# Optimization experiments

Hardware: AMD Instinct MI355X
Metric: run time of the kernel (lower is better)

The kernel has to match this reference:

```python
import jax, jax.numpy as jnp
import numpy as np

N, E, O, C, D_IN, OUT, L, B = 10000, 80000, 10, 64, 16, 16, 2, 16
DEG, WIDEN, BD = 3, 4, 64
EPS = 1e-6


def fibonacci_sphere(n):
    # deterministic near-uniform grid of n unit vectors on S^2 (stands in for GridGenerator's repulsion grid)
    i = jnp.arange(n, dtype=jnp.float32) + 0.5
    phi = jnp.arccos(1.0 - 2.0 * i / n)
    theta = jnp.pi * (1.0 + 5.0 ** 0.5) * i
    return jnp.stack([jnp.cos(theta) * jnp.sin(phi), jnp.sin(theta) * jnp.sin(phi), jnp.cos(phi)], axis=-1)


def poly_features(x, degree):
    # PolynomialFeatures: concat x, x(x)x, x(x)x(x)x, ... flattened outer products
    feats = [x]
    cur = x
    for _ in range(degree):
        cur = (cur[..., :, None] * x[..., None, :]).reshape(x.shape[:-1] + (-1,))
        feats.append(cur)
    return jnp.concatenate(feats, axis=-1)


def layer_norm(x, scale, bias):
    mu = jnp.mean(x, axis=-1, keepdims=True)
    var = jnp.mean((x - mu) ** 2, axis=-1, keepdims=True)
    return (x - mu) * jax.lax.rsqrt(var + EPS) * scale + bias


def setup_inputs():
    key = jax.random.key(0)
    ks = jax.random.split(key, 16)
    def w(k, shape):
        return jax.random.normal(k, shape, dtype=jnp.float32) / np.sqrt(shape[-2])
    P_SP = 2 + 4 + 8 + 16  # poly features of 2-dim spatial invariants, degree 3
    P_OR = 4               # poly features of 1-dim orientation invariant, degree 3
    return {
        "x": jax.random.normal(ks[0], (N, D_IN), jnp.float32),
        "pos": jax.random.normal(ks[1], (N, 3), jnp.float32),
        "basis_w1": w(ks[2], (P_SP, C)), "basis_b1": jnp.zeros((C,), jnp.float32),
        "basis_w2": w(ks[3], (C, BD)), "basis_b2": jnp.zeros((BD,), jnp.float32),
        "fbasis_w1": w(ks[4], (P_OR, C)), "fbasis_b1": jnp.zeros((C,), jnp.float32),
        "fbasis_w2": w(ks[5], (C, BD)), "fbasis_b2": jnp.zeros((BD,), jnp.float32),
        "embed_w": w(ks[6], (D_IN, C)),
        "conv_kw": w(ks[7], (L, BD, C)),
        "conv_fw": w(ks[8], (L, BD, C)),
        "conv_b": jnp.zeros((L, C), jnp.float32),
        "norm_s": jnp.ones((L, C), jnp.float32),
        "norm_b": jnp.zeros((L, C), jnp.float32),
        "lin1_w": w(ks[9], (L, C, WIDEN * C)), "lin1_b": jnp.zeros((L, WIDEN * C), jnp.float32),
        "lin2_w": w(ks[10], (L, WIDEN * C, C)), "lin2_b": jnp.zeros((L, C), jnp.float32),
        "ro_w": w(ks[11], (L, C, OUT)), "ro_b": jnp.zeros((L, OUT), jnp.float32),
        "edge_index": jax.random.randint(ks[12], (2, E), 0, N, jnp.int32),
        "batch": jnp.sort(jax.random.randint(ks[13], (N,), 0, B, jnp.int32)),
    }


def reference(x, pos, basis_w1, basis_b1, basis_w2, basis_b2, fbasis_w1, fbasis_b1, fbasis_w2, fbasis_b2, embed_w, conv_kw, conv_fw, conv_b, norm_s, norm_b, lin1_w, lin1_b, lin2_w, lin2_b, ro_w, ro_b, edge_index, batch):
    ori = fibonacci_sphere(O)                                             # [O,3]
    send, recv = edge_index[0], edge_index[1]
    rel = (pos[send] - pos[recv])[:, None, :]                              # [E,1,3]
    inv1 = jnp.sum(rel * ori[None], axis=-1, keepdims=True)                # [E,O,1]
    inv2 = jnp.linalg.norm(rel - inv1 * ori[None], axis=-1, keepdims=True) # [E,O,1]
    inv3 = jnp.sum(ori[None, :, :] * ori[:, None, :], axis=-1, keepdims=True)  # [O,O,1]
    sp = jnp.concatenate([inv1, inv2], axis=-1)                            # [E,O,2]
    kb = jax.nn.gelu(poly_features(sp, DEG) @ basis_w1 + basis_b1)
    kb = jax.nn.gelu(kb @ basis_w2 + basis_b2)                             # [E,O,BD]
    fkb = jax.nn.gelu(poly_features(inv3, DEG) @ fbasis_w1 + fbasis_b1)
    fkb = jax.nn.gelu(fkb @ fbasis_w2 + fbasis_b2)                         # [O,O,BD]
    h = jnp.broadcast_to((x @ embed_w)[:, None, :], (N, O, C))             # [N,O,C]
    readout = jnp.zeros((N, O, OUT), h.dtype)
    for l in range(L):
        # depthwise spatial conv: gather-send, modulate by kernel, scatter-add to receivers
        msg = h[send] * (kb @ conv_kw[l])                                  # [E,O,C]
        h1 = jax.ops.segment_sum(msg, recv, num_segments=N)                # [N,O,C]
        # depthwise fiber (orientation) conv
        fk = fkb @ conv_fw[l]                                              # [O,O,C]
        h2 = jnp.einsum('noc,poc->npc', h1, fk) / O + conv_b[l]
        # ConvNeXt MLP + residual
        y = layer_norm(h2, norm_s[l], norm_b[l])
        y = jax.nn.gelu(y @ lin1_w[l] + lin1_b[l]) @ lin2_w[l] + lin2_b[l]
        h = h + y
        readout = readout + (h @ ro_w[l] + ro_b[l])
    readout = readout / L
    out_scalar = jnp.mean(readout, axis=-2)                                # [N,OUT]
    pooled = jnp.zeros((B, OUT), out_scalar.dtype).at[batch].add(out_scalar)
    return pooled
```

## Files before the change

### kernel.cpp

```cpp
#include <hip/hip_runtime.h>
#include <math.h>

#define N_   10000
#define E_   80000
#define O_   10
#define B_   16
#define OUT_ 16
#define NROW_ (N_*O_)
#define NITEM_ (E_*O_)

typedef __attribute__((ext_vector_type(8))) short bf16x8;
typedef __attribute__((ext_vector_type(4))) short bf16x4;
typedef __attribute__((ext_vector_type(4))) float f32x4;

#define MFMA16(a,b,c) __builtin_amdgcn_mfma_f32_16x16x32_bf16(a,b,c,0,0,0)

__device__ __forceinline__ float gelu_f(float x) {
    float u = fmaf(0.044715f, x * x, 1.0f);
    float e = __builtin_amdgcn_exp2f(2.3022083f * x * u);
    float r = __builtin_amdgcn_rcpf(e + 1.0f);
    return fmaf(-x, r, x);
}

__device__ __forceinline__ unsigned short f2bf(float f) {
    union { float f; unsigned int u; } v; v.f = f;
    unsigned int r = v.u + 0x7FFFu + ((v.u >> 16) & 1u);
    return (unsigned short)(r >> 16);
}
__device__ __forceinline__ float bf2f(unsigned short u) {
    union { unsigned int u; float f; } v; v.u = ((unsigned int)u) << 16;
    return v.f;
}
__device__ __forceinline__ unsigned int cvtpk(float lo, float hi) {
    unsigned int r;
    asm("v_cvt_pk_bf16_f32 %0, %1, %2" : "=v"(r) : "v"(lo), "v"(hi));
    return r;
}
__device__ __forceinline__ bf16x4 pack4(float a, float b, float c, float d) {
    union { unsigned int u[2]; bf16x4 v; } z;
    z.u[0] = cvtpk(a, b);
    z.u[1] = cvtpk(c, d);
    return z.v;
}

__device__ __forceinline__ void fib_vec(int idx, float& vx, float& vy, float& vz) {
    float i = (float)idx + 0.5f;
    float phi = acosf(1.0f - 2.0f * i / (float)O_);
    float theta = 3.14159265358979323846f * (1.0f + 2.2360679774997896964f) * i;
    float sp = sinf(phi);
    vx = cosf(theta) * sp; vy = sinf(theta) * sp; vz = cosf(phi);
}

__global__ __launch_bounds__(256) void k_pack(
    const float* __restrict__ bw1, const float* __restrict__ bw2,
    const float* __restrict__ ckw, const float* __restrict__ l1w,
    const float* __restrict__ l2w, const float* __restrict__ row_w,
    float* __restrict__ orig,
    unsigned short* __restrict__ wW1P, unsigned short* __restrict__ wW2P,
    unsigned short* __restrict__ wCKP, unsigned short* __restrict__ wL1P,
    unsigned short* __restrict__ wL2P, unsigned short* __restrict__ wROP)
{
    const int g = blockIdx.x * 256 + threadIdx.x;
    if (g < 2048) {
        int idx = g;
        int t = idx >> 9, rem = idx & 511;
        int ln = rem >> 3, j = rem & 7;
        int row = t*16 + (ln & 15);
        int k = (ln >> 4)*8 + j;
        float s = 0.0f;
        if (k < 14) {
            const int moff[14] = {0,1,2,3,5,6,7,10,13,14,15,19,25,29};
            const int mcnt[14] = {1,1,1,2,1,1,3,3,1,1,4,6,4,1};
            const int mlist[30] = {0,1,2,3,4,5,6,7,8,10,9,11,12,13,14,
                                   15,16,18,22,17,19,20,23,24,26,21,25,27,28,29};
            for (int q = 0; q < mcnt[k]; ++q) s += bw1[mlist[moff[k]+q]*64 + row];
        }
        wW1P[idx] = f2bf(s);
    } else if (g < 6144) {
        int idx = g - 2048;
        int t = idx >> 9, rem = idx & 511;
        int mt = t >> 1, ks = t & 1;
        int ln = rem >> 3, j = rem & 7;
        int row = mt*16 + (ln & 15);
        int k = ks*32 + (ln >> 4)*8 + j;
        wW2P[idx] = f2bf(bw2[k*64 + row]);
    } else if (g < 14336) {
        int idx = g - 6144;
        int l = idx >> 12, r2 = idx & 4095;
        int t = r2 >> 9, rem = r2 & 511;
        int mt = t >> 1, ks = t & 1;
        int ln = rem >> 3, j = rem & 7;
        int row = mt*16 + (ln & 15);
        int k = ks*32 + (ln >> 4)*8 + j;
        wCKP[idx] = f2bf(ckw[l*4096 + k*64 + row]);
    } else if (g < 47104) {
        int idx = g - 14336;
        int l = idx >> 14, r2 = idx & 16383;
        int t = r2 >> 9, rem = r2 & 511;
        int mt = t >> 1, ks = t & 1;
        int ln = rem >> 3, j = rem & 7;
        int row = mt*16 + (ln & 15);
        int k = ks*32 + (ln >> 4)*8 + j;
        wL1P[idx] = f2bf(l1w[l*16384 + k*256 + row]);
    } else if (g < 79872) {
        int idx = g - 47104;
        int l = idx >> 14, r2 = idx & 16383;
        int t = r2 >> 9, rem = r2 & 511;
        int mt2 = t >> 3, ksg = t & 7;
        int ln = rem >> 3, j = rem & 7;
        int row = mt2*16 + (ln & 15);
        int k = ksg*32 + (ln >> 4)*8 + j;
        wL2P[idx] = f2bf(l2w[l*16384 + k*64 + row]);
    } else if (g < 81920) {
        int idx = g - 79872;
        int l = idx >> 10, r2 = idx & 1023;
        int ks = r2 >> 9, rem = r2 & 511;
        int ln = rem >> 3, j = rem & 7;
        int row = ln & 15;
        int k = ks*32 + (ln >> 4)*8 + j;
        wROP[idx] = f2bf(row_w[l*1024 + k*16 + row]);
    } else if (g < 81920 + O_) {
        int o = g - 81920;
        float vx, vy, vz;
        fib_vec(o, vx, vy, vz);
        orig[o*3+0] = vx; orig[o*3+1] = vy; orig[o*3+2] = vz;
    }
}

__global__ __launch_bounds__(256) void k_fibpre(
    const float* __restrict__ fw1, const float* __restrict__ fb1,
    const float* __restrict__ fw2, const float* __restrict__ fb2,
    const float* __restrict__ cfw, float* __restrict__ fkg)
{
    __shared__ float sRow[4][64];
    const int wv = threadIdx.x >> 6, lane = threadIdx.x & 63;
    const int pr = blockIdx.x * 4 + wv;
    if (pr >= 100) return;
    const int i = pr / O_, j = pr % O_;
    float ix, iy, iz, jx, jy, jz;
    fib_vec(i, ix, iy, iz);
    fib_vec(j, jx, jy, jz);
    float a = ix*jx + iy*jy + iz*jz;
    float a2 = a*a, a3 = a2*a, a4 = a3*a;
    float v = fb1[lane];
    v = fmaf(a,  fw1[0*64+lane], v);
    v = fmaf(a2, fw1[1*64+lane], v);
    v = fmaf(a3, fw1[2*64+lane], v);
    v = fmaf(a4, fw1[3*64+lane], v);
    sRow[wv][lane] = gelu_f(v);
    float acc = fb2[lane];
    for (int b = 0; b < 64; ++b) acc = fmaf(sRow[wv][b], fw2[b*64+lane], acc);
    sRow[wv][lane] = gelu_f(acc);
    for (int l = 0; l < 2; ++l) {
        float s = 0.0f;
        for (int b = 0; b < 64; ++b) s = fmaf(sRow[wv][b], cfw[l*4096 + b*64 + lane], s);
        fkg[l*6400 + pr*64 + lane] = s;
    }
}

__global__ __launch_bounds__(256) void k_embed(
    const float* __restrict__ x, const float* __restrict__ ew,
    float* __restrict__ hg, unsigned short* __restrict__ hbf0)
{
    int t = blockIdx.x * 256 + threadIdx.x;
    if (t >= N_ * 64) return;
    int n = t >> 6, c = t & 63;
    float v = 0.0f;
#pragma unroll
    for (int k = 0; k < 16; ++k) v = fmaf(x[n*16+k], ew[k*64+c], v);
    int base = n * 640 + c;
#pragma unroll
    for (int o = 0; o < O_; ++o) hg[base + o*64] = v;
    hbf0[t] = f2bf(v);
}

__global__ __launch_bounds__(256) void k_hist(const int* __restrict__ ei, int* __restrict__ counts)
{
    int e = blockIdx.x * 256 + threadIdx.x;
    if (e < E_) atomicAdd(&counts[ei[E_ + e]], 1);
}

__global__ __launch_bounds__(1024) void k_scan(
    const int* __restrict__ counts, int* __restrict__ offs, int* __restrict__ cursor)
{
    __shared__ int part[1024];
    int t = threadIdx.x;
    const int CH = 10;
    int base_i = t * CH;
    int s = 0;
#pragma unroll
    for (int i = 0; i < CH; ++i) { int idx = base_i + i; if (idx < N_) s += counts[idx]; }
    part[t] = s;
    __syncthreads();
    for (int off = 1; off < 1024; off <<= 1) {
        int v = (t >= off) ? part[t - off] : 0;
        __syncthreads();
        part[t] += v;
        __syncthreads();
    }
    int run = (t > 0) ? part[t - 1] : 0;
#pragma unroll
    for (int i = 0; i < CH; ++i) {
        int idx = base_i + i;
        if (idx < N_) { offs[idx] = run; cursor[idx] = run; run += counts[idx]; }
    }
    if (t == 1023) offs[N_] = run;
}

__global__ __launch_bounds__(256) void k_scatter(
    const int* __restrict__ ei, const float* __restrict__ pos,
    int* __restrict__ cursor, int* __restrict__ csend, int* __restrict__ crecv,
    float* __restrict__ crel)
{
    int e = blockIdx.x * 256 + threadIdx.x;
    if (e >= E_) return;
    int s = ei[e], r = ei[E_ + e];
    int slot = atomicAdd(&cursor[r], 1);
    csend[slot] = s;
    crecv[slot] = r;
    crel[slot*3+0] = pos[s*3+0] - pos[r*3+0];
    crel[slot*3+1] = pos[s*3+1] - pos[r*3+1];
    crel[slot*3+2] = pos[s*3+2] - pos[r*3+2];
}

template<int KS>
__device__ __forceinline__ void loadB(
    const unsigned short* sData, int lane, bf16x8 Bf[4][KS])
{
    const int lm = lane & 15, lk = lane >> 4;
#pragma unroll
    for (int nt = 0; nt < 4; ++nt)
#pragma unroll
        for (int ks = 0; ks < KS; ++ks) {
            int r = nt*16 + lm;
            int kb = ks*64 + lk*16;
            Bf[nt][ks] = *(const bf16x8*)((const char*)sData + r*128 + (kb ^ ((r&7)<<4)));
        }
}

template<int KS, bool BIAS, bool GELU>
__device__ __forceinline__ void stageC(
    unsigned short* sData, const bf16x8 Bf[4][KS],
    const unsigned short* __restrict__ Wp, const float* __restrict__ bias, int lane)
{
    const int lm = lane & 15, lk = lane >> 4;
#pragma unroll
    for (int mt = 0; mt < 4; ++mt) {
        bf16x8 Af[KS];
#pragma unroll
        for (int ks = 0; ks < KS; ++ks)
            Af[ks] = *(const bf16x8*)(Wp + ((mt*KS + ks)*64 + lane)*8);
        f32x4 b4 = {0,0,0,0};
        if (BIAS) b4 = *(const f32x4*)(bias + mt*16 + (lk<<2));
#pragma unroll
        for (int nt = 0; nt < 4; ++nt) {
            f32x4 acc = b4;
#pragma unroll
            for (int ks = 0; ks < KS; ++ks) acc = MFMA16(Af[ks], Bf[nt][ks], acc);
            float v0 = acc[0], v1 = acc[1], v2 = acc[2], v3 = acc[3];
            if (GELU) { v0 = gelu_f(v0); v1 = gelu_f(v1); v2 = gelu_f(v2); v3 = gelu_f(v3); }
            bf16x4 pk = pack4(v0, v1, v2, v3);
            int rr = nt*16 + lm;
            int cb = mt*32 + (lk<<3);
            *(bf16x4*)((char*)sData + rr*128 + (cb ^ ((rr&7)<<4))) = pk;
        }
    }
}

__device__ __forceinline__ void phase0(
    unsigned short* sData, int slot, int oo, const float* __restrict__ crel,
    const float* __restrict__ ori, int tid)
{
    float r0 = crel[slot*3+0], r1 = crel[slot*3+1], r2 = crel[slot*3+2];
    float o0 = ori[oo*3+0], o1 = ori[oo*3+1], o2 = ori[oo*3+2];
    float a = r0*o0 + r1*o1 + r2*o2;
    float p0 = fmaf(-a, o0, r0), p1 = fmaf(-a, o1, r1), p2 = fmaf(-a, o2, r2);
    float b = sqrtf(p0*p0 + p1*p1 + p2*p2);
    float a2 = a*a, b2 = b*b, ab = a*b;
    float m[14];
    m[0]=a; m[1]=b; m[2]=a2; m[3]=ab; m[4]=b2;
    m[5]=a2*a; m[6]=a2*b; m[7]=a*b2; m[8]=b2*b;
    m[9]=a2*a2; m[10]=a2*ab; m[11]=a2*b2; m[12]=ab*b2; m[13]=b2*b2;
    unsigned int pk[16];
#pragma unroll
    for (int j = 0; j < 7; ++j) pk[j] = cvtpk(m[2*j], m[2*j+1]);
#pragma unroll
    for (int j = 7; j < 16; ++j) pk[j] = 0;
#pragma unroll
    for (int q = 0; q < 4; ++q) {
        int cb = q*16;
        *(f32x4*)((char*)sData + tid*128 + (cb ^ ((tid&7)<<4))) = ((const f32x4*)pk)[q];
    }
}

#define SCATTER_BODY(KC_EXPR)                                                        \
    int prevr = __shfl_up(rcv, 1);                                                   \
    unsigned long long bmask = __ballot(lane > 0 && rcv != prevr);                   \
    float a0=0,a1c=0,a2c=0,a3c=0,a4c=0,a5c=0,a6c=0,a7c=0,a8c=0,a9c=0;                \
    int cur = __builtin_amdgcn_readfirstlane(rcv);                                   \
    int soi = item0 % 10;                                                            \
    _Pragma("unroll")                                                                \
    for (int ch = 0; ch < 4; ++ch) {                                                 \
        unsigned short hvu[16]; float kcv[16];                                       \
        _Pragma("unroll")                                                            \
        for (int j = 0; j < 16; ++j) {                                               \
            const int i = ch*16 + j;                                                 \
            hvu[j] = hb[__builtin_amdgcn_readlane(myaddr, i)];                       \
            kcv[j] = (KC_EXPR);                                                      \
        }                                                                            \
        _Pragma("unroll")                                                            \
        for (int j = 0; j < 16; ++j) {                                               \
            const int i = ch*16 + j;                                                 \
            if (bmask & (1ull << i)) { FLUSH_RUN(cur); cur = __builtin_amdgcn_readlane(rcv, i); } \
            float mv = kcv[j] * bf2f(hvu[j]);                                        \
            if      (soi == 0) a0  += mv;                                            \
            else if (soi == 1) a1c += mv;                                            \
            else if (soi == 2) a2c += mv;                                            \
            else if (soi == 3) a3c += mv;                                            \
            else if (soi == 4) a4c += mv;                                            \
            else if (soi == 5) a5c += mv;                                            \
            else if (soi == 6) a6c += mv;                                            \
            else if (soi == 7) a7c += mv;                                            \
            else if (soi == 8) a8c += mv;                                            \
            else               a9c += mv;                                            \
            soi = (soi == 9) ? 0 : soi + 1;                                          \
        }                                                                            \
    }                                                                                \
    FLUSH_RUN(cur);

#define FLUSH_RUN(R) { float* bp = h1g + (R)*640 + lane; \
    atomicAdd(bp+0,a0); atomicAdd(bp+64,a1c); atomicAdd(bp+128,a2c); atomicAdd(bp+192,a3c); \
    atomicAdd(bp+256,a4c); atomicAdd(bp+320,a5c); atomicAdd(bp+384,a6c); atomicAdd(bp+448,a7c); \
    atomicAdd(bp+512,a8c); atomicAdd(bp+576,a9c); \
    a0=a1c=a2c=a3c=a4c=a5c=a6c=a7c=a8c=a9c=0.0f; }

template<bool L0>
__global__ __launch_bounds__(64) void k_msg(
    const unsigned short* __restrict__ hbf, float* __restrict__ h1g,
    const int* __restrict__ csend, const int* __restrict__ crecv,
    const float* __restrict__ crel, const float* __restrict__ ori,
    const unsigned short* __restrict__ wW1P, const unsigned short* __restrict__ wW2P,
    const unsigned short* __restrict__ wCKP_l,
    const float* __restrict__ bb1, const float* __restrict__ bb2)
{
    __shared__ unsigned short sData[64*64];
    const int lane = threadIdx.x;
    const int item0 = blockIdx.x * 64;
    const int item = item0 + lane;
    const int slot = item / 10;
    const int oo = item - slot * 10;
    const int snd = csend[slot];
    const int rcv = crecv[slot];
    phase0(sData, slot, oo, crel, ori, lane);
    {
        bf16x8 Bf1[4][1]; loadB<1>(sData, lane, Bf1);
        stageC<1, true, true>(sData, Bf1, wW1P, bb1, lane);
    }
    {
        bf16x8 Bf2[4][2]; loadB<2>(sData, lane, Bf2);
        stageC<2, true, true>(sData, Bf2, wW2P, bb2, lane);
    }
    {
        bf16x8 Bf3[4][2]; loadB<2>(sData, lane, Bf3);
        stageC<2, false, false>(sData, Bf3, wCKP_l, (const float*)0, lane);
    }
    const int myaddr = L0 ? (snd * 64) : ((snd * 10 + oo) * 64);
    const unsigned short* hb = hbf + lane;
    SCATTER_BODY(bf2f(*(const unsigned short*)((const char*)sData + i*128 + ((lane*2) ^ ((i&7)<<4)))))
}

__global__ __launch_bounds__(64) void k_msg0dual(
    const unsigned short* __restrict__ hbf, float* __restrict__ h1g,
    unsigned short* __restrict__ kc1g,
    const int* __restrict__ csend, const int* __restrict__ crecv,
    const float* __restrict__ crel, const float* __restrict__ ori,
    const unsigned short* __restrict__ wW1P, const unsigned short* __restrict__ wW2P,
    const unsigned short* __restrict__ wCK0, const unsigned short* __restrict__ wCK1,
    const float* __restrict__ bb1, const float* __restrict__ bb2)
{
    __shared__ unsigned short sData[64*64];
    const int lane = threadIdx.x;
    const int item0 = blockIdx.x * 64;
    const int item = item0 + lane;
    const int slot = item / 10;
    const int oo = item - slot * 10;
    const int snd = csend[slot];
    const int rcv = crecv[slot];
    phase0(sData, slot, oo, crel, ori, lane);
    {
        bf16x8 Bf1[4][1]; loadB<1>(sData, lane, Bf1);
        stageC<1, true, true>(sData, Bf1, wW1P, bb1, lane);
    }
    {
        bf16x8 Bf2[4][2]; loadB<2>(sData, lane, Bf2);
        stageC<2, true, true>(sData, Bf2, wW2P, bb2, lane);
    }
    bf16x8 Bf3[4][2]; loadB<2>(sData, lane, Bf3);
    stageC<2, false, false>(sData, Bf3, wCK1, (const float*)0, lane);
    {
        char* dst = (char*)kc1g + (size_t)item0 * 128;
#pragma unroll
        for (int q = 0; q < 8; ++q) {
            int g = q*1024 + lane*16;
            int row = g >> 7;
            int off = g & 127;
            f32x4 v = *(const f32x4*)((const char*)sData + row*128 + (off ^ ((row&7)<<4)));
            *(f32x4*)(dst + g) = v;
        }
    }
    stageC<2, false, false>(sData, Bf3, wCK0, (const float*)0, lane);
    const int myaddr = snd * 64;
    const unsigned short* hb = hbf + lane;
    SCATTER_BODY(bf2f(*(const unsigned short*)((const char*)sData + i*128 + ((lane*2) ^ ((i&7)<<4)))))
}

__global__ __launch_bounds__(64) void k_msg1lite(
    const unsigned short* __restrict__ kc1g, const unsigned short* __restrict__ hbf,
    float* __restrict__ h1g,
    const int* __restrict__ csend, const int* __restrict__ crecv)
{
    const int lane = threadIdx.x;
    const int item0 = blockIdx.x * 64;
    const int item = item0 + lane;
    const int slot = item / 10;
    const int oo = item - slot * 10;
    const int snd = csend[slot];
    const int rcv = crecv[slot];
    const int myaddr = (snd * 10 + oo) * 64;
    const unsigned short* hb = hbf + lane;
    const char* kb = (const char*)kc1g + (size_t)item0 * 128;
    SCATTER_BODY(bf2f(*(const unsigned short*)(kb + (size_t)i*128 + lane*2)))
}
#undef FLUSH_RUN
#undef SCATTER_BODY

__global__ __launch_bounds__(256) void k_fln(
    float* __restrict__ h1, const float* __restrict__ fkg,
    const float* __restrict__ cb, const float* __restrict__ ns,
    const float* __restrict__ nb, unsigned short* __restrict__ y, int zero_h1)
{
    __shared__ float sFK[6400];
    const int tid = threadIdx.x;
    for (int i = tid; i < 6400; i += 256) sFK[i] = fkg[i];
    __syncthreads();
    const int lane = tid & 63, wv = tid >> 6;
    float cbv = cb[lane], nsv = ns[lane], nbv = nb[lane];
    for (int g4 = blockIdx.x; g4 < N_/4; g4 += gridDim.x) {
        const int n = g4 * 4 + wv;
        float hr[10];
#pragma unroll
        for (int o = 0; o < O_; ++o) hr[o] = h1[n*640 + o*64 + lane];
        if (zero_h1) {
#pragma unroll
            for (int o = 0; o < O_; ++o) h1[n*640 + o*64 + lane] = 0.0f;
        }
#pragma unroll
        for (int p = 0; p < O_; ++p) {
            float v = 0.0f;
#pragma unroll
            for (int o = 0; o < O_; ++o) v = fmaf(hr[o], sFK[(p*O_+o)*64 + lane], v);
            v = v * 0.1f + cbv;
            float s = v, q = v*v;
#pragma unroll
            for (int d = 1; d < 64; d <<= 1) { s += __shfl_xor(s, d); q += __shfl_xor(q, d); }
            float mu = s * (1.0f/64.0f);
            float var = q * (1.0f/64.0f) - mu*mu;
            float rs = rsqrtf(var + 1e-6f);
            float yv = (v - mu) * rs * nsv + nbv;
            y[(n*O_ + p)*64 + lane] = f2bf(yv);
        }
    }
}

__global__ __launch_bounds__(256, 3) void k_mlp(
    unsigned short* ybuf, float* __restrict__ hg, float* __restrict__ rout,
    const unsigned short* __restrict__ wL1P_l, const float* __restrict__ l1b_l,
    const unsigned short* __restrict__ wL2P_l, const float* __restrict__ l2b_l,
    const unsigned short* __restrict__ wROP_l, const float* __restrict__ rob_l)
{
    __shared__ unsigned short sA[128*64];
    const int tid = threadIdx.x;
    const int lane = tid & 63, wv = tid >> 6;
    const int rb = blockIdx.x * 128;
#pragma unroll
    for (int i = tid*16; i < 128*128; i += 256*16) {
        int r = i >> 7, off = i & 127;
        int grow = rb + r; if (grow >= NROW_) grow = NROW_ - 1;
        *(f32x4*)((char*)sA + r*128 + (off ^ ((r&7)<<4))) =
            *(const f32x4*)((const char*)ybuf + (size_t)grow*128 + off);
    }
    __syncthreads();
    const int lm = lane & 15, lk = lane >> 4;
    bf16x8 Yf[2][2];
#pragma unroll
    for (int nt = 0; nt < 2; ++nt)
#pragma unroll
        for (int ks = 0; ks < 2; ++ks) {
            int r = wv*32 + nt*16 + lm;
            int kb = ks*64 + lk*16;
            Yf[nt][ks] = *(const bf16x8*)((const char*)sA + r*128 + (kb ^ ((r&7)<<4)));
        }
    f32x4 acc2[4][2];
#pragma unroll
    for (int m = 0; m < 4; ++m) {
        f32x4 b2 = *(const f32x4*)(l2b_l + m*16 + (lk<<2));
#pragma unroll
        for (int nt = 0; nt < 2; ++nt) acc2[m][nt] = b2;
    }
#pragma unroll
    for (int jb = 0; jb < 4; ++jb) {
#pragma unroll
        for (int mt = 0; mt < 4; ++mt) {
            bf16x8 A1[2];
#pragma unroll
            for (int ks = 0; ks < 2; ++ks)
                A1[ks] = *(const bf16x8*)(wL1P_l + (((jb*4 + mt)*2 + ks)*64 + lane)*8);
            f32x4 b4 = *(const f32x4*)(l1b_l + jb*64 + mt*16 + (lk<<2));
#pragma unroll
            for (int nt = 0; nt < 2; ++nt) {
                f32x4 acc = b4;
                acc = MFMA16(A1[0], Yf[nt][0], acc);
                acc = MFMA16(A1[1], Yf[nt][1], acc);
                bf16x4 pk = pack4(gelu_f(acc[0]), gelu_f(acc[1]), gelu_f(acc[2]), gelu_f(acc[3]));
                int rr = wv*32 + nt*16 + lm;
                int cb = mt*32 + (lk<<3);
                *(bf16x4*)((char*)sA + rr*128 + (cb ^ ((rr&7)<<4))) = pk;
            }
        }
        bf16x8 Mf[2][2];
#pragma unroll
        for (int nt = 0; nt < 2; ++nt)
#pragma unroll
            for (int ks = 0; ks < 2; ++ks) {
                int r = wv*32 + nt*16 + lm;
                int kb = ks*64 + lk*16;
                Mf[nt][ks] = *(const bf16x8*)((const char*)sA + r*128 + (kb ^ ((r&7)<<4)));
            }
#pragma unroll
        for (int mt2 = 0; mt2 < 4; ++mt2) {
            bf16x8 A2[2];
#pragma unroll
            for (int ks = 0; ks < 2; ++ks)
                A2[ks] = *(const bf16x8*)(wL2P_l + ((mt2*8 + jb*2 + ks)*64 + lane)*8);
#pragma unroll
            for (int nt = 0; nt < 2; ++nt) {
                acc2[mt2][nt] = MFMA16(A2[0], Mf[nt][0], acc2[mt2][nt]);
                acc2[mt2][nt] = MFMA16(A2[1], Mf[nt][1], acc2[mt2][nt]);
            }
        }
    }
#pragma unroll
    for (int nt = 0; nt < 2; ++nt) {
        const int rloc = wv*32 + nt*16 + lm;
        const int grow = rb + rloc;
        const bool valid = grow < NROW_;
        const int growc = valid ? grow : (NROW_ - 1);
#pragma unroll
        for (int mt2 = 0; mt2 < 4; ++mt2) {
            f32x4 hv = *(const f32x4*)(hg + (size_t)growc*64 + mt2*16 + (lk<<2));
            f32x4 hn;
#pragma unroll
            for (int r = 0; r < 4; ++r) hn[r] = hv[r] + acc2[mt2][nt][r];
            bf16x4 pk = pack4(hn[0], hn[1], hn[2], hn[3]);
            if (valid) {
                *(f32x4*)(hg + (size_t)grow*64 + mt2*16 + (lk<<2)) = hn;
                *(bf16x4*)((char*)ybuf + (size_t)grow*128 + (mt2*16 + (lk<<2))*2) = pk;
            }
            int cb = mt2*32 + (lk<<3);
            *(bf16x4*)((char*)sA + rloc*128 + (cb ^ ((rloc&7)<<4))) = pk;
        }
    }
    bf16x8 Ro[2];
#pragma unroll
    for (int ks = 0; ks < 2; ++ks)
        Ro[ks] = *(const bf16x8*)(wROP_l + (ks*64 + lane)*8);
    f32x4 rb4 = *(const f32x4*)(rob_l + (lk<<2));
#pragma unroll
    for (int nt = 0; nt < 2; ++nt) {
        const int rloc = wv*32 + nt*16 + lm;
        const int grow = rb + rloc;
        bf16x8 Hf[2];
#pragma unroll
        for (int ks = 0; ks < 2; ++ks) {
            int kb = ks*64 + lk*16;
            Hf[ks] = *(const bf16x8*)((const char*)sA + rloc*128 + (kb ^ ((rloc&7)<<4)));
        }
        f32x4 r4 = rb4;
        r4 = MFMA16(Ro[0], Hf[0], r4);
        r4 = MFMA16(Ro[1], Hf[1], r4);
        if (grow < NROW_) *(f32x4*)(rout + (size_t)grow*16 + (lk<<2)) = r4;
    }
}

__global__ __launch_bounds__(256) void k_pool(
    const float* __restrict__ r0, const float* __restrict__ r1,
    const int* __restrict__ batch, float* __restrict__ out)
{
    int t = blockIdx.x * 256 + threadIdx.x;
    if (t >= N_ * 16) return;
    int n = t >> 4, j = t & 15;
    float s = 0.0f;
#pragma unroll
    for (int p = 0; p < O_; ++p)
        s += r0[(n*O_ + p)*16 + j] + r1[(n*O_ + p)*16 + j];
    atomicAdd(&out[batch[n]*16 + j], s * (1.0f/20.0f));
}

extern "C" void kernel_launch(void* const* d_in, const int* in_sizes, int n_in,
                              void* d_out, int out_size, void* d_ws, size_t ws_size,
                              hipStream_t stream)
{
    const float* x    = (const float*)d_in[0];
    const float* pos  = (const float*)d_in[1];
    const float* bw1  = (const float*)d_in[2];
    const float* bb1  = (const float*)d_in[3];
    const float* bw2  = (const float*)d_in[4];
    const float* bb2  = (const float*)d_in[5];
    const float* fw1  = (const float*)d_in[6];
    const float* fb1  = (const float*)d_in[7];
    const float* fw2  = (const float*)d_in[8];
    const float* fb2  = (const float*)d_in[9];
    const float* embw = (const float*)d_in[10];
    const float* ckw  = (const float*)d_in[11];
    const float* cfw  = (const float*)d_in[12];
    const float* cb   = (const float*)d_in[13];
    const float* ns   = (const float*)d_in[14];
    const float* nbp  = (const float*)d_in[15];
    const float* l1w  = (const float*)d_in[16];
    const float* l1b  = (const float*)d_in[17];
    const float* l2w  = (const float*)d_in[18];
    const float* l2b  = (const float*)d_in[19];
    const float* row  = (const float*)d_in[20];
    const float* rob  = (const float*)d_in[21];
    const int*   ei   = (const int*)d_in[22];
    const int*   batch= (const int*)d_in[23];
    float* out = (float*)d_out;

    char* w = (char*)d_ws;
    size_t off = 0;
    auto alloc = [&](size_t bytes) -> char* {
        char* p = w + off; off += (bytes + 255) / 256 * 256; return p;
    };
    float* ori    = (float*)alloc(32 * 4);
    float* fkg    = (float*)alloc(2 * 6400 * 4);
    unsigned short* wW1P = (unsigned short*)alloc(4*512*2);
    unsigned short* wW2P = (unsigned short*)alloc(8*512*2);
    unsigned short* wCKP = (unsigned short*)alloc(2*8*512*2);
    unsigned short* wL1P = (unsigned short*)alloc(2*32*512*2);
    unsigned short* wL2P = (unsigned short*)alloc(2*32*512*2);
    unsigned short* wROP = (unsigned short*)alloc(2*2*512*2);
    float* h      = (float*)alloc((size_t)N_ * 640 * 4);
    float* h1     = (float*)alloc((size_t)N_ * 640 * 4);
    unsigned short* y = (unsigned short*)alloc((size_t)NROW_ * 64 * 2);
    unsigned short* hbf0 = (unsigned short*)alloc((size_t)N_ * 64 * 2);
    float* rout0  = (float*)alloc((size_t)NROW_ * 16 * 4);
    float* rout1  = (float*)alloc((size_t)NROW_ * 16 * 4);
    float* crel   = (float*)alloc((size_t)E_ * 3 * 4);
    int*   counts = (int*)alloc((N_ + 1) * 4);
    int*   offs   = (int*)alloc((N_ + 1) * 4);
    int*   cursor = (int*)alloc((N_ + 1) * 4);
    int*   csend  = (int*)alloc((size_t)E_ * 4);
    int*   crecv  = (int*)alloc((size_t)E_ * 4);
    unsigned short* kc1g = nullptr;
    if (ws_size >= off + (size_t)NITEM_ * 64 * 2 + 256)
        kc1g = (unsigned short*)alloc((size_t)NITEM_ * 64 * 2);

    hipMemsetAsync(h1, 0, (size_t)N_ * 640 * 4, stream);
    hipMemsetAsync(out, 0, (size_t)out_size * 4, stream);
    hipMemsetAsync(counts, 0, (N_ + 1) * 4, stream);

    k_pack<<<321, 256, 0, stream>>>(bw1, bw2, ckw, l1w, l2w, row, ori,
                                    wW1P, wW2P, wCKP, wL1P, wL2P, wROP);
    k_fibpre<<<25, 256, 0, stream>>>(fw1, fb1, fw2, fb2, cfw, fkg);
    k_embed<<<(N_ * 64 + 255) / 256, 256, 0, stream>>>(x, embw, h, hbf0);
    k_hist<<<(E_ + 255) / 256, 256, 0, stream>>>(ei, counts);
    k_scan<<<1, 1024, 0, stream>>>(counts, offs, cursor);
    k_scatter<<<(E_ + 255) / 256, 256, 0, stream>>>(ei, pos, cursor, csend, crecv, crel);

    for (int l = 0; l < 2; ++l) {
        if (l == 0) {
            if (kc1g)
                k_msg0dual<<<NITEM_ / 64, 64, 0, stream>>>(hbf0, h1, kc1g, csend, crecv,
                                                           crel, ori, wW1P, wW2P,
                                                           wCKP, wCKP + 4096, bb1, bb2);
            else
                k_msg<true><<<NITEM_ / 64, 64, 0, stream>>>(hbf0, h1, csend, crecv, crel, ori,
                                                            wW1P, wW2P, wCKP, bb1, bb2);
        } else {
            if (kc1g)
                k_msg1lite<<<NITEM_ / 64, 64, 0, stream>>>(kc1g, y, h1, csend, crecv);
            else
                k_msg<false><<<NITEM_ / 64, 64, 0, stream>>>(y, h1, csend, crecv, crel, ori,
                                                             wW1P, wW2P, wCKP + 4096, bb1, bb2);
        }
        k_fln<<<625, 256, 0, stream>>>(h1, fkg + l*6400, cb + l*64, ns + l*64, nbp + l*64, y,
                                       (l == 0) ? 1 : 0);
        k_mlp<<<(NROW_ + 127) / 128, 256, 0, stream>>>(y, h, (l == 0 ? rout0 : rout1),
                                                       wL1P + l*16384, l1b + l*256,
                                                       wL2P + l*16384, l2b + l*64,
                                                       wROP + l*1024, rob + l*16);
    }
    k_pool<<<(N_ * 16 + 255) / 256, 256, 0, stream>>>(rout0, rout1, batch, out);
}
```

Measured before the change: 406.1 us.

## Precompute swizzle pointers, flatten fln grid, skip last-layer h writes, raise mlp occupancy

Several independent micro-optimizations. The scatter bodies use eight precomputed swizzled LDS base pointers instead of recomputing the XOR address each iteration, and the per-lane offset in msg1lite is hoisted. k_fln now launches one block per four nodes instead of a grid-stride loop over 625 blocks, which reloads the fiber kernel into shared memory in every one of those blocks. k_mlp is templated so the last layer skips writing back h and the bf16 copy that nothing reads afterwards, and its launch bound asks for four blocks per SM, which may cause register spills.

```diff
diff --git a/kernel.cpp b/kernel.cpp
--- a/kernel.cpp
+++ b/kernel.cpp
@@ -366,7 +366,10 @@
     }
     const int myaddr = L0 ? (snd * 64) : ((snd * 10 + oo) * 64);
     const unsigned short* hb = hbf + lane;
-    SCATTER_BODY(bf2f(*(const unsigned short*)((const char*)sData + i*128 + ((lane*2) ^ ((i&7)<<4)))))
+    const char* vb[8];
+#pragma unroll
+    for (int k = 0; k < 8; ++k) vb[k] = (const char*)sData + ((lane*2) ^ (k<<4));
+    SCATTER_BODY(bf2f(*(const unsigned short*)(vb[j&7] + i*128)))
 }
 
 __global__ __launch_bounds__(64) void k_msg0dual(
@@ -411,7 +414,10 @@
     stageC<2, false, false>(sData, Bf3, wCK0, (const float*)0, lane);
     const int myaddr = snd * 64;
     const unsigned short* hb = hbf + lane;
-    SCATTER_BODY(bf2f(*(const unsigned short*)((const char*)sData + i*128 + ((lane*2) ^ ((i&7)<<4)))))
+    const char* vb[8];
+#pragma unroll
+    for (int k = 0; k < 8; ++k) vb[k] = (const char*)sData + ((lane*2) ^ (k<<4));
+    SCATTER_BODY(bf2f(*(const unsigned short*)(vb[j&7] + i*128)))
 }
 
 __global__ __launch_bounds__(64) void k_msg1lite(
@@ -428,8 +434,8 @@
     const int rcv = crecv[slot];
     const int myaddr = (snd * 10 + oo) * 64;
     const unsigned short* hb = hbf + lane;
-    const char* kb = (const char*)kc1g + (size_t)item0 * 128;
-    SCATTER_BODY(bf2f(*(const unsigned short*)(kb + (size_t)i*128 + lane*2)))
+    const char* kb = (const char*)kc1g + (size_t)item0 * 128 + lane*2;
+    SCATTER_BODY(bf2f(*(const unsigned short*)(kb + (size_t)i*128)))
 }
 #undef FLUSH_RUN
 #undef SCATTER_BODY
@@ -445,34 +451,33 @@
     __syncthreads();
     const int lane = tid & 63, wv = tid >> 6;
     float cbv = cb[lane], nsv = ns[lane], nbv = nb[lane];
-    for (int g4 = blockIdx.x; g4 < N_/4; g4 += gridDim.x) {
-        const int n = g4 * 4 + wv;
-        float hr[10];
-#pragma unroll
-        for (int o = 0; o < O_; ++o) hr[o] = h1[n*640 + o*64 + lane];
-        if (zero_h1) {
-#pragma unroll
-            for (int o = 0; o < O_; ++o) h1[n*640 + o*64 + lane] = 0.0f;
-        }
-#pragma unroll
-        for (int p = 0; p < O_; ++p) {
-            float v = 0.0f;
-#pragma unroll
-            for (int o = 0; o < O_; ++o) v = fmaf(hr[o], sFK[(p*O_+o)*64 + lane], v);
-            v = v * 0.1f + cbv;
-            float s = v, q = v*v;
-#pragma unroll
-            for (int d = 1; d < 64; d <<= 1) { s += __shfl_xor(s, d); q += __shfl_xor(q, d); }
-            float mu = s * (1.0f/64.0f);
-            float var = q * (1.0f/64.0f) - mu*mu;
-            float rs = rsqrtf(var + 1e-6f);
-            float yv = (v - mu) * rs * nsv + nbv;
-            y[(n*O_ + p)*64 + lane] = f2bf(yv);
-        }
-    }
-}
-
-__global__ __launch_bounds__(256, 3) void k_mlp(
+    const int n = blockIdx.x * 4 + wv;
+    float hr[10];
+#pragma unroll
+    for (int o = 0; o < O_; ++o) hr[o] = h1[n*640 + o*64 + lane];
+    if (zero_h1) {
+#pragma unroll
+        for (int o = 0; o < O_; ++o) h1[n*640 + o*64 + lane] = 0.0f;
+    }
+#pragma unroll
+    for (int p = 0; p < O_; ++p) {
+        float v = 0.0f;
+#pragma unroll
+        for (int o = 0; o < O_; ++o) v = fmaf(hr[o], sFK[(p*O_+o)*64 + lane], v);
+        v = v * 0.1f + cbv;
+        float s = v, q = v*v;
+#pragma unroll
+        for (int d = 1; d < 64; d <<= 1) { s += __shfl_xor(s, d); q += __shfl_xor(q, d); }
+        float mu = s * (1.0f/64.0f);
+        float var = q * (1.0f/64.0f) - mu*mu;
+        float rs = rsqrtf(var + 1e-6f);
+        float yv = (v - mu) * rs * nsv + nbv;
+        y[(n*O_ + p)*64 + lane] = f2bf(yv);
+    }
+}
+
+template<int LAST>
+__global__ __launch_bounds__(256, 4) void k_mlp(
     unsigned short* ybuf, float* __restrict__ hg, float* __restrict__ rout,
     const unsigned short* __restrict__ wL1P_l, const float* __restrict__ l1b_l,
     const unsigned short* __restrict__ wL2P_l, const float* __restrict__ l2b_l,
@@ -562,7 +567,7 @@
 #pragma unroll
             for (int r = 0; r < 4; ++r) hn[r] = hv[r] + acc2[mt2][nt][r];
             bf16x4 pk = pack4(hn[0], hn[1], hn[2], hn[3]);
-            if (valid) {
+            if (!LAST && valid) {
                 *(f32x4*)(hg + (size_t)grow*64 + mt2*16 + (lk<<2)) = hn;
                 *(bf16x4*)((char*)ybuf + (size_t)grow*128 + (mt2*16 + (lk<<2))*2) = pk;
             }
@@ -693,12 +698,17 @@
                 k_msg<false><<<NITEM_ / 64, 64, 0, stream>>>(y, h1, csend, crecv, crel, ori,
                                                              wW1P, wW2P, wCKP + 4096, bb1, bb2);
         }
-        k_fln<<<625, 256, 0, stream>>>(h1, fkg + l*6400, cb + l*64, ns + l*64, nbp + l*64, y,
-                                       (l == 0) ? 1 : 0);
-        k_mlp<<<(NROW_ + 127) / 128, 256, 0, stream>>>(y, h, (l == 0 ? rout0 : rout1),
-                                                       wL1P + l*16384, l1b + l*256,
-                                                       wL2P + l*16384, l2b + l*64,
-                                                       wROP + l*1024, rob + l*16);
+        k_fln<<<N_ / 4, 256, 0, stream>>>(h1, fkg + l*6400, cb + l*64, ns + l*64, nbp + l*64, y,
+                                          (l == 0) ? 1 : 0);
+        if (l == 0)
+            k_mlp<0><<<(NROW_ + 127) / 128, 256, 0, stream>>>(y, h, rout0,
+                                                              wL1P, l1b, wL2P, l2b,
+                                                              wROP, rob);
+        else
+            k_mlp<1><<<(NROW_ + 127) / 128, 256, 0, stream>>>(y, h, rout1,
+                                                              wL1P + 16384, l1b + 256,
+                                                              wL2P + 16384, l2b + 64,
+                                                              wROP + 1024, rob + 16);
     }
     k_pool<<<(N_ * 16 + 255) / 256, 256, 0, stream>>>(rout0, rout1, batch, out);
 }
```

After: 397.0 us. -2.2%, faster.
